# Kernel tuning notes

Hardware: AMD Instinct MI355X
Metric: run time of the kernel (lower is better)

The kernel has to match this reference:

```python
import jax, jax.numpy as jnp
import numpy as np

N = 50000
IN_CHNL = 128
OUT_CHNL = 64
HEADS = 2
NEG_SLOPE = 0.2  # PyG GATConv default leaky_relu slope


def gat_conv(x, W, a_src, a_dst, bias, edge_index):
    """PyG-style GATConv (concat=True, add_self_loops=True, eval mode).
    x: [N, F_in], W: [F_in, H*C], a_src/a_dst: [H, C], bias: [H*C],
    edge_index: [2, E] (row 0 = src, row 1 = dst)."""
    n = x.shape[0]
    loops = jnp.arange(n, dtype=edge_index.dtype)
    src = jnp.concatenate([edge_index[0], loops])
    dst = jnp.concatenate([edge_index[1], loops])

    h = (x @ W).reshape(n, HEADS, OUT_CHNL)          # [N, H, C]
    s_src = jnp.einsum('nhc,hc->nh', h, a_src)       # [N, H]
    s_dst = jnp.einsum('nhc,hc->nh', h, a_dst)       # [N, H]

    e = s_src[src] + s_dst[dst]                      # [E', H]
    e = jax.nn.leaky_relu(e, NEG_SLOPE)
    # segment softmax over destination neighborhoods
    e_max = jax.ops.segment_max(e, dst, num_segments=n)
    e_max = jnp.where(jnp.isfinite(e_max), e_max, 0.0)
    e_exp = jnp.exp(e - e_max[dst])
    denom = jax.ops.segment_sum(e_exp, dst, num_segments=n)
    alpha = e_exp / denom[dst]                       # [E', H]

    msg = h[src] * alpha[:, :, None]                 # [E', H, C]
    out = jax.ops.segment_sum(msg, dst, num_segments=n)  # [N, H, C]
    return out.reshape(n, HEADS * OUT_CHNL) + bias


def setup_inputs() -> dict:
    key = jax.random.key(0)
    ks = jax.random.split(key, 12)
    node_h = jax.random.normal(ks[0], (N, IN_CHNL), dtype=jnp.float32)
    edge_index_pc = jax.random.randint(ks[1], (2, 600000), 0, N, dtype=jnp.int64 if jax.config.jax_enable_x64 else jnp.int32)
    edge_index_mc = jax.random.randint(ks[2], (2, 600000), 0, N, dtype=jnp.int64 if jax.config.jax_enable_x64 else jnp.int32)
    sc = 1.0 / np.sqrt(IN_CHNL)
    W_pc = jax.random.normal(ks[3], (IN_CHNL, HEADS * OUT_CHNL), dtype=jnp.float32) * sc
    a_src_pc = jax.random.normal(ks[4], (HEADS, OUT_CHNL), dtype=jnp.float32) * sc
    a_dst_pc = jax.random.normal(ks[5], (HEADS, OUT_CHNL), dtype=jnp.float32) * sc
    b_pc = jnp.zeros((HEADS * OUT_CHNL,), dtype=jnp.float32)
    W_mc = jax.random.normal(ks[6], (IN_CHNL, HEADS * OUT_CHNL), dtype=jnp.float32) * sc
    a_src_mc = jax.random.normal(ks[7], (HEADS, OUT_CHNL), dtype=jnp.float32) * sc
    a_dst_mc = jax.random.normal(ks[8], (HEADS, OUT_CHNL), dtype=jnp.float32) * sc
    b_mc = jnp.zeros((HEADS * OUT_CHNL,), dtype=jnp.float32)
    return {
        'node_h': node_h,
        'W_pc': W_pc, 'a_src_pc': a_src_pc, 'a_dst_pc': a_dst_pc, 'b_pc': b_pc,
        'W_mc': W_mc, 'a_src_mc': a_src_mc, 'a_dst_mc': a_dst_mc, 'b_mc': b_mc,
        'edge_index_pc': edge_index_pc, 'edge_index_mc': edge_index_mc,
    }


def reference(node_h, W_pc, a_src_pc, a_dst_pc, b_pc,
              W_mc, a_src_mc, a_dst_mc, b_mc,
              edge_index_pc, edge_index_mc):
    # eval mode: F.dropout is identity
    h_pc = jax.nn.elu(gat_conv(node_h, W_pc, a_src_pc, a_dst_pc, b_pc, edge_index_pc))
    h_mc = jax.nn.elu(gat_conv(node_h, W_mc, a_src_mc, a_dst_mc, b_mc, edge_index_mc))
    return 0.5 * (h_pc + h_mc)
```

## Files before the change

### kernel.cpp

```cpp
#include <hip/hip_runtime.h>
#include <hip/hip_bf16.h>

typedef unsigned int u32;
typedef unsigned short u16;
typedef long long i64;
typedef __bf16 bf16x8 __attribute__((ext_vector_type(8)));
typedef float f32x4 __attribute__((ext_vector_type(4)));

static constexpr int NN = 50000;
static constexpr int FI = 128;
static constexpr int FO = 128;
static constexpr int ER = 600000;
static constexpr int GLAB = 6272;
static constexpr int PROWS = 12544;
static constexpr int DSTRIDE = 38;
static constexpr int NQA = 640;
static constexpr int ACS = (2 * ER) / NQA;
static constexpr int NBIN = 128;
static constexpr int RBLK = 784;
static constexpr int LCAP = 64;
static constexpr int QCAPB = 10240;
static constexpr float SLOPE = 0.2f;

__device__ __forceinline__ float bf2f(u16 u) {
  u32 x = ((u32)u) << 16;
  return __builtin_bit_cast(float, x);
}
__device__ __forceinline__ u16 f2bf(float f) {
  u32 u = __builtin_bit_cast(u32, f);
  u32 r = (u + 0x7fffu + ((u >> 16) & 1u)) >> 16;
  return (u16)r;
}
__device__ __forceinline__ float ldf(const void* p, size_t i, int isf32) {
  return isf32 ? ((const float*)p)[i] : bf2f(((const u16*)p)[i]);
}
__device__ __forceinline__ int lde(const void* p, size_t i, int is64) {
  return is64 ? (int)((const i64*)p)[i] : ((const int*)p)[i];
}

__global__ void wfrag_prep(const void* __restrict__ W0,
                           const void* __restrict__ W1,
                           const u32* __restrict__ x,
                           const u32* __restrict__ ei, u16* __restrict__ wf,
                           int* __restrict__ flags, int* __restrict__ qcur) {
  int lane = threadIdx.x;
  u32 e = (x[lane] >> 23) & 0xffu;
  unsigned long long b1 = __ballot(e >= 118u && e <= 137u);
  int f32i = (__popcll(b1) >= 48) ? 1 : 0;
  int bid = blockIdx.x;
  if (bid == 64) {
    if (lane < 64) {
      u32 hi = (lane < 32) ? ei[2 * lane + 1] : 1u;
      unsigned long long b2 = __ballot(hi == 0u);
      if (lane == 0) {
        flags[0] = f32i;
        flags[1] = (__popcll(b2) >= 30) ? 1 : 0;
      }
    }
    if (lane < NBIN - 64) qcur[64 + lane] = 0;
    if (lane < 64) qcur[lane] = 0;
    return;
  }
  int g = bid >> 5, idx = bid & 31;
  const void* W = g ? W1 : W0;
  int ks = idx >> 3, cg = idx & 7;
  int k0 = ks * 32 + (lane >> 4) * 8;
  int col = cg * 16 + (lane & 15);
  u16 v[8];
#pragma unroll
  for (int j = 0; j < 8; j++) v[j] = f2bf(ldf(W, (size_t)(k0 + j) * FO + col, f32i));
  u32 p0 = (u32)v[0] | ((u32)v[1] << 16);
  u32 p1 = (u32)v[2] | ((u32)v[3] << 16);
  u32 p2 = (u32)v[4] | ((u32)v[5] << 16);
  u32 p3 = (u32)v[6] | ((u32)v[7] << 16);
  *reinterpret_cast<uint4*>(wf + (size_t)(bid * 64 + lane) * 8) =
      make_uint4(p0, p1, p2, p3);
}

__device__ __forceinline__ void gemm_body(
    const void* __restrict__ x, const u16* __restrict__ wf,
    u16* __restrict__ h0, u16* __restrict__ h1, const void* __restrict__ as0,
    const void* __restrict__ ad0, const void* __restrict__ as1,
    const void* __restrict__ ad1, float* __restrict__ ss,
    float* __restrict__ sd, int f32i, int bid) {
  int tid = threadIdx.x;
  int lane = tid & 63;
  int wv = tid >> 6;
  int rowbase = bid * 64 + wv * 16;
  int arow = rowbase + (lane & 15);
  if (arow >= NN) arow = NN - 1;
  int kg = lane >> 4;

  f32x4 acc[16];
#pragma unroll
  for (int i = 0; i < 16; i++) acc[i] = (f32x4){0.f, 0.f, 0.f, 0.f};

#pragma unroll
  for (int ks = 0; ks < 4; ks++) {
    uint4 q;
    if (f32i) {
      const float* xp = (const float*)x + (size_t)arow * FI + ks * 32 + kg * 8;
      float4 v0 = *reinterpret_cast<const float4*>(xp);
      float4 v1 = *reinterpret_cast<const float4*>(xp + 4);
      q.x = (u32)f2bf(v0.x) | ((u32)f2bf(v0.y) << 16);
      q.y = (u32)f2bf(v0.z) | ((u32)f2bf(v0.w) << 16);
      q.z = (u32)f2bf(v1.x) | ((u32)f2bf(v1.y) << 16);
      q.w = (u32)f2bf(v1.z) | ((u32)f2bf(v1.w) << 16);
    } else {
      q = *reinterpret_cast<const uint4*>((const u16*)x + (size_t)arow * FI +
                                          ks * 32 + kg * 8);
    }
    bf16x8 a = __builtin_bit_cast(bf16x8, q);
#pragma unroll
    for (int cg = 0; cg < 16; cg++) {
      int g = cg >> 3;
      bf16x8 b = __builtin_bit_cast(
          bf16x8,
          *reinterpret_cast<const uint4*>(
              wf + (size_t)((g * 32 + ks * 8 + (cg & 7)) * 64 + lane) * 8));
      acc[cg] = __builtin_amdgcn_mfma_f32_16x16x32_bf16(a, b, acc[cg], 0, 0, 0);
    }
  }
#pragma unroll
  for (int cg = 0; cg < 16; cg++) {
    u16* h = (cg < 8) ? h0 : h1;
#pragma unroll
    for (int r = 0; r < 4; r++) {
      int orow = rowbase + kg * 4 + r;
      if (orow < NN)
        h[(size_t)orow * FO + (cg & 7) * 16 + (lane & 15)] = f2bf(acc[cg][r]);
    }
  }
  float sa[4][4], sb[4][4];
#pragma unroll
  for (int i = 0; i < 4; i++)
#pragma unroll
    for (int r = 0; r < 4; r++) {
      sa[i][r] = 0.f;
      sb[i][r] = 0.f;
    }
#pragma unroll
  for (int cg = 0; cg < 16; cg++) {
    int c = (cg & 7) * 16 + (lane & 15);
    const void* as = (cg < 8) ? as0 : as1;
    const void* ad = (cg < 8) ? ad0 : ad1;
    float av = ldf(as, c, f32i);
    float dv = ldf(ad, c, f32i);
    int ih = cg >> 2;
#pragma unroll
    for (int r = 0; r < 4; r++) {
      sa[ih][r] += acc[cg][r] * av;
      sb[ih][r] += acc[cg][r] * dv;
    }
  }
#pragma unroll
  for (int i = 0; i < 4; i++)
#pragma unroll
    for (int r = 0; r < 4; r++)
#pragma unroll
      for (int off = 1; off <= 8; off <<= 1) {
        sa[i][r] += __shfl_xor(sa[i][r], off, 64);
        sb[i][r] += __shfl_xor(sb[i][r], off, 64);
      }
  if ((lane & 15) < 8) {
    int r = lane & 3;
    int g = (lane >> 2) & 1;
    int row = rowbase + kg * 4 + r;
    if (row < NN) {
      reinterpret_cast<float2*>(ss)[(size_t)g * NN + row] =
          make_float2(sa[g * 2][r], sa[g * 2 + 1][r]);
      reinterpret_cast<float2*>(sd)[(size_t)g * NN + row] =
          make_float2(sb[g * 2][r], sb[g * 2 + 1][r]);
    }
  }
}

__device__ __forceinline__ void passA_body(const void* __restrict__ ei0,
                                           const void* __restrict__ ei1,
                                           int* __restrict__ qcur,
                                           u32* __restrict__ qbuf,
                                           const int* __restrict__ flags,
                                           int bid) {
  __shared__ u32 lq[NBIN][LCAP];
  __shared__ int lcnt[NBIN];
  __shared__ int gbase[NBIN];
  int tid = threadIdx.x;
  if (tid < NBIN) lcnt[tid] = 0;
  __syncthreads();
  int i64f = flags[1];
  int beg = bid * ACS;
  int end = beg + ACS;
  for (int e = beg + tid; e < end; e += 256) {
    int g = e >= ER;
    int ee = e - g * ER;
    const void* ei = g ? ei1 : ei0;
    int d = lde(ei, (size_t)ER + ee, i64f);
    int s = lde(ei, (size_t)ee, i64f);
    s = min(max(s, 0), NN - 1);
    d = min(max(d, 0), NN - 1);
    int p = d & 7;
    int label = (d >> 3) + g * GLAB;
    int r = label / RBLK;
    int bin = p * 16 + r;
    int ll = label - r * RBLK;
    int pos = atomicAdd(&lcnt[bin], 1);
    if (pos < LCAP) lq[bin][pos] = ((u32)s << 16) | (u32)ll;
  }
  __syncthreads();
  if (tid < NBIN) {
    int n = min(lcnt[tid], LCAP);
    lcnt[tid] = n;
    gbase[tid] = atomicAdd(&qcur[tid], n);
  }
  __syncthreads();
  int wv = tid >> 6, lane = tid & 63;
  for (int b = wv; b < NBIN; b += 4) {
    int n = lcnt[b];
    int gb = gbase[b];
    for (int i = lane; i < n; i += 64) {
      int idx = gb + i;
      if (idx < QCAPB) qbuf[(size_t)b * QCAPB + idx] = lq[b][i];
    }
  }
}

__global__ __launch_bounds__(256) void fat1(
    const void* __restrict__ x, const u16* __restrict__ wf,
    u16* __restrict__ h0, u16* __restrict__ h1, const void* __restrict__ as0,
    const void* __restrict__ ad0, const void* __restrict__ as1,
    const void* __restrict__ ad1, float* __restrict__ ss,
    float* __restrict__ sd, const void* __restrict__ ei0,
    const void* __restrict__ ei1, int* __restrict__ qcur,
    u32* __restrict__ qbuf, const int* __restrict__ flags) {
  if (blockIdx.x < NQA) {
    passA_body(ei0, ei1, qcur, qbuf, flags, blockIdx.x);
  } else {
    gemm_body(x, wf, h0, h1, as0, ad0, as1, ad1, ss, sd, flags[0],
              blockIdx.x - NQA);
  }
}

__global__ __launch_bounds__(256) void passB(const int* __restrict__ qcur,
                                             const u32* __restrict__ qbuf,
                                             int* __restrict__ deg,
                                             u16* __restrict__ slots) {
  __shared__ int ldeg[RBLK];
  __shared__ u16 lslots[RBLK * DSTRIDE];
  int tid = threadIdx.x;
  int bin = blockIdx.x;
  int p = bin >> 4, r = bin & 15;
  for (int i = tid; i < RBLK; i += 256) {
    int lgl = r * RBLK + i;
    int g = lgl >= GLAB;
    int lg = lgl - g * GLAB;
    int dst = (lg << 3) | p;
    if (dst < NN) {
      ldeg[i] = 1;
      lslots[i * DSTRIDE] = (u16)dst;
    } else {
      ldeg[i] = 0;
    }
  }
  __syncthreads();
  int qn = min(qcur[bin], QCAPB);
  const u32* q = qbuf + (size_t)bin * QCAPB;
  for (int i = tid; i < qn; i += 256) {
    u32 pr = q[i];
    int ll = (int)(pr & 0xffffu);
    int old = atomicAdd(&ldeg[ll], 1);
    if (old < DSTRIDE) lslots[ll * DSTRIDE + old] = (u16)(pr >> 16);
  }
  __syncthreads();
  int rowbase = p * PROWS + r * RBLK;
  for (int i = tid; i < RBLK; i += 256) deg[rowbase + i] = min(ldeg[i], DSTRIDE);
  const u32* ls32 = reinterpret_cast<const u32*>(lslots);
  u32* gs32 = reinterpret_cast<u32*>(slots + (size_t)rowbase * DSTRIDE);
  for (int i = tid; i < RBLK * DSTRIDE / 2; i += 256) gs32[i] = ls32[i];
}

__global__ __launch_bounds__(256) void agg2(
    const u16* __restrict__ h0, const u16* __restrict__ h1,
    const float* __restrict__ ss, const float* __restrict__ sd,
    const int* __restrict__ deg, const u16* __restrict__ slots,
    const void* __restrict__ b0p, const void* __restrict__ b1p,
    void* __restrict__ outp, const int* __restrict__ flags) {
  int f32i = flags[0];
  int tid = threadIdx.x;
  int lane = tid & 63, wv = tid >> 6;
  int half = lane >> 5;
  int c = lane & 31;
  int dst = blockIdx.x * 8 + wv * 2 + half;
  int head = c >> 4;
  int hsh = head << 4;
  int hbase = half << 5;
  float res[2][4];
#pragma unroll
  for (int g = 0; g < 2; g++) {
    const uint2* hw = reinterpret_cast<const uint2*>(g ? h1 : h0);
    const float2* ss2 = reinterpret_cast<const float2*>(ss) + (size_t)g * NN;
    float2 sdv = reinterpret_cast<const float2*>(sd)[(size_t)g * NN + dst];
    int row = (dst & 7) * PROWS + g * GLAB + (dst >> 3);
    int n = min(deg[row], DSTRIDE);
    const u16* srow = slots + (size_t)row * DSTRIDE;
    int n1 = min(n, 32);
    int s1 = 0, s2 = 0;
    u32 pp1 = 0, pp2 = 0;
    float dp0 = 0.f, dp1 = 0.f;
    if (c < n1) {
      s1 = srow[c];
      float2 sv = ss2[s1];
      float e0 = sv.x + sdv.x, e1 = sv.y + sdv.y;
      e0 = (e0 > 0.f) ? e0 : SLOPE * e0;
      e1 = (e1 > 0.f) ? e1 : SLOPE * e1;
      float q0 = __expf(e0), q1 = __expf(e1);
      pp1 = (u32)f2bf(q0) | ((u32)f2bf(q1) << 16);
      dp0 += q0;
      dp1 += q1;
    }
    if (c + 32 < n) {
      s2 = srow[c + 32];
      float2 sv = ss2[s2];
      float e0 = sv.x + sdv.x, e1 = sv.y + sdv.y;
      e0 = (e0 > 0.f) ? e0 : SLOPE * e0;
      e1 = (e1 > 0.f) ? e1 : SLOPE * e1;
      float q0 = __expf(e0), q1 = __expf(e1);
      pp2 = (u32)f2bf(q0) | ((u32)f2bf(q1) << 16);
      dp0 += q0;
      dp1 += q1;
    }
#pragma unroll
    for (int off = 16; off >= 1; off >>= 1) {
      dp0 += __shfl_xor(dp0, off, 32);
      dp1 += __shfl_xor(dp1, off, 32);
    }
    float den = head ? dp1 : dp0;
    float a0 = 0.f, a1 = 0.f, a2 = 0.f, a3 = 0.f;
    int n1full = n1 & ~7;
    for (int b = 0; b < n1full; b += 8) {
      uint2 hv[8];
      float pv[8];
#pragma unroll
      for (int t = 0; t < 8; t++) {
        int sj = __shfl(s1, hbase + b + t, 64);
        u32 pp = __shfl(pp1, hbase + b + t, 64);
        pv[t] = bf2f((u16)(pp >> hsh));
        hv[t] = hw[(size_t)sj * 32 + c];
      }
#pragma unroll
      for (int t = 0; t < 8; t++) {
        a0 += pv[t] * bf2f((u16)hv[t].x);
        a1 += pv[t] * bf2f((u16)(hv[t].x >> 16));
        a2 += pv[t] * bf2f((u16)hv[t].y);
        a3 += pv[t] * bf2f((u16)(hv[t].y >> 16));
      }
    }
    if (n1full < n1) {
      uint2 hv[8];
      float pv[8];
#pragma unroll
      for (int t = 0; t < 8; t++) {
        int jj = (n1full + t < n1) ? (n1full + t) : n1full;
        int sj = __shfl(s1, hbase + jj, 64);
        u32 pp = __shfl(pp1, hbase + jj, 64);
        pv[t] = (n1full + t < n1) ? bf2f((u16)(pp >> hsh)) : 0.f;
        hv[t] = hw[(size_t)sj * 32 + c];
      }
#pragma unroll
      for (int t = 0; t < 8; t++) {
        a0 += pv[t] * bf2f((u16)hv[t].x);
        a1 += pv[t] * bf2f((u16)(hv[t].x >> 16));
        a2 += pv[t] * bf2f((u16)hv[t].y);
        a3 += pv[t] * bf2f((u16)(hv[t].y >> 16));
      }
    }
    if (n > 32) {
      int n2 = n - 32;
      for (int b = 0; b < n2; b += 8) {
        uint2 hv[8];
        float pv[8];
#pragma unroll
        for (int t = 0; t < 8; t++) {
          int jj = (b + t < n2) ? (b + t) : b;
          int sj = __shfl(s2, hbase + jj, 64);
          u32 pp = __shfl(pp2, hbase + jj, 64);
          pv[t] = (b + t < n2) ? bf2f((u16)(pp >> hsh)) : 0.f;
          hv[t] = hw[(size_t)sj * 32 + c];
        }
#pragma unroll
        for (int t = 0; t < 8; t++) {
          a0 += pv[t] * bf2f((u16)hv[t].x);
          a1 += pv[t] * bf2f((u16)(hv[t].x >> 16));
          a2 += pv[t] * bf2f((u16)hv[t].y);
          a3 += pv[t] * bf2f((u16)(hv[t].y >> 16));
        }
      }
    }
    float inv = (den > 0.f) ? 1.0f / den : 0.f;
    const void* bias = g ? b1p : b0p;
    float r0 = a0 * inv + ldf(bias, 4 * c + 0, f32i);
    float r1 = a1 * inv + ldf(bias, 4 * c + 1, f32i);
    float r2 = a2 * inv + ldf(bias, 4 * c + 2, f32i);
    float r3 = a3 * inv + ldf(bias, 4 * c + 3, f32i);
    res[g][0] = (r0 > 0.f) ? r0 : (__expf(r0) - 1.0f);
    res[g][1] = (r1 > 0.f) ? r1 : (__expf(r1) - 1.0f);
    res[g][2] = (r2 > 0.f) ? r2 : (__expf(r2) - 1.0f);
    res[g][3] = (r3 > 0.f) ? r3 : (__expf(r3) - 1.0f);
  }
  float r0 = 0.5f * (res[0][0] + res[1][0]);
  float r1 = 0.5f * (res[0][1] + res[1][1]);
  float r2 = 0.5f * (res[0][2] + res[1][2]);
  float r3 = 0.5f * (res[0][3] + res[1][3]);
  if (f32i) {
    reinterpret_cast<float4*>(outp)[(size_t)dst * 32 + c] =
        make_float4(r0, r1, r2, r3);
  } else {
    uint2 o;
    o.x = (u32)f2bf(r0) | ((u32)f2bf(r1) << 16);
    o.y = (u32)f2bf(r2) | ((u32)f2bf(r3) << 16);
    reinterpret_cast<uint2*>(outp)[(size_t)dst * 32 + c] = o;
  }
}

extern "C" void kernel_launch(void* const* d_in, const int* in_sizes, int n_in,
                              void* d_out, int out_size, void* d_ws, size_t ws_size,
                              hipStream_t stream) {
  (void)in_sizes; (void)n_in; (void)out_size; (void)ws_size;
  const void* x = d_in[0];

  char* base = (char*)d_ws;
  size_t off = 0;
  auto alloc = [&](size_t bytes) -> void* {
    void* p = base + off;
    off = (off + bytes + 255) & ~(size_t)255;
    return p;
  };
  int* flags = (int*)alloc(16);
  int* qcur  = (int*)alloc(NBIN * 4);
  u16* h0    = (u16*)alloc((size_t)NN * FO * 2);
  u16* h1    = (u16*)alloc((size_t)NN * FO * 2);
  float* ss  = (float*)alloc((size_t)2 * NN * 2 * 4);
  float* sd  = (float*)alloc((size_t)2 * NN * 2 * 4);
  u16* wf    = (u16*)alloc((size_t)2 * 32 * 64 * 8 * 2);
  int* deg   = (int*)alloc((size_t)8 * PROWS * 4);
  u16* slots = (u16*)alloc((size_t)8 * PROWS * DSTRIDE * 2);
  u32* qbuf  = (u32*)alloc((size_t)NBIN * QCAPB * 4);

  const int GEMM_BLK = (NN + 63) / 64;
  const int AGG_BLK = NN / 8;

  wfrag_prep<<<65, 64, 0, stream>>>(d_in[1], d_in[5], (const u32*)x,
                                    (const u32*)d_in[9], wf, flags, qcur);
  fat1<<<NQA + GEMM_BLK, 256, 0, stream>>>(x, wf, h0, h1, d_in[2], d_in[3],
                                           d_in[6], d_in[7], ss, sd, d_in[9],
                                           d_in[10], qcur, qbuf, flags);
  passB<<<NBIN, 256, 0, stream>>>(qcur, qbuf, deg, slots);
  agg2<<<AGG_BLK, 256, 0, stream>>>(h0, h1, ss, sd, deg, slots, d_in[4],
                                    d_in[8], d_out, flags);
}
```

Measured before the change: 130.7 us.

## Restructure pre-aggregation stages: merge weight prep with edge binning, split GEMM per layer

Weight-fragment prep and the edge-binning pass now share one launch, so binning no longer depends on a prior flag kernel. The GEMM moves to its own launch with one block per layer per row tile, which halves accumulator registers per block and doubles block count. Edge binning uses twice as many blocks and a smaller per-block shared queue, with overflow going straight to global atomics. The per-bin counters are padded to separate cache lines and cleared by a memset. The trade-off is an extra kernel launch and a memset in exchange for better occupancy and less counter contention.

```diff
diff --git a/kernel.cpp b/kernel.cpp
--- a/kernel.cpp
+++ b/kernel.cpp
@@ -14,12 +14,13 @@
 static constexpr int GLAB = 6272;
 static constexpr int PROWS = 12544;
 static constexpr int DSTRIDE = 38;
-static constexpr int NQA = 640;
-static constexpr int ACS = (2 * ER) / NQA;
+static constexpr int NQA = 1280;
+static constexpr int ACS = (2 * ER + NQA - 1) / NQA;
 static constexpr int NBIN = 128;
 static constexpr int RBLK = 784;
-static constexpr int LCAP = 64;
+static constexpr int LCAP = 24;
 static constexpr int QCAPB = 10240;
+static constexpr int GEMM_BLK = (NN + 63) / 64;
 static constexpr float SLOPE = 0.2f;
 
 __device__ __forceinline__ float bf2f(u16 u) {
@@ -38,62 +39,128 @@
   return is64 ? (int)((const i64*)p)[i] : ((const int*)p)[i];
 }
 
-__global__ void wfrag_prep(const void* __restrict__ W0,
-                           const void* __restrict__ W1,
-                           const u32* __restrict__ x,
-                           const u32* __restrict__ ei, u16* __restrict__ wf,
-                           int* __restrict__ flags, int* __restrict__ qcur) {
-  int lane = threadIdx.x;
-  u32 e = (x[lane] >> 23) & 0xffu;
-  unsigned long long b1 = __ballot(e >= 118u && e <= 137u);
-  int f32i = (__popcll(b1) >= 48) ? 1 : 0;
+__device__ __forceinline__ void passA_body(const void* __restrict__ ei0,
+                                           const void* __restrict__ ei1,
+                                           int* __restrict__ qcurp,
+                                           u32* __restrict__ qbuf, int bid) {
+  __shared__ u32 lq[NBIN][LCAP];
+  __shared__ int lcnt[NBIN];
+  __shared__ int gbase[NBIN];
+  __shared__ int s_i64;
+  int tid = threadIdx.x;
+  if (tid < NBIN) lcnt[tid] = 0;
+  if (tid < 64) {
+    u32 hi = (tid < 32) ? ((const u32*)ei0)[2 * tid + 1] : 1u;
+    unsigned long long b2 = __ballot(hi == 0u);
+    if (tid == 0) s_i64 = (__popcll(b2) >= 30) ? 1 : 0;
+  }
+  __syncthreads();
+  int i64f = s_i64;
+  int beg = bid * ACS;
+  int end = min(beg + ACS, 2 * ER);
+  for (int e = beg + tid; e < end; e += 256) {
+    int g = e >= ER;
+    int ee = e - g * ER;
+    const void* ei = g ? ei1 : ei0;
+    int d = lde(ei, (size_t)ER + ee, i64f);
+    int s = lde(ei, (size_t)ee, i64f);
+    s = min(max(s, 0), NN - 1);
+    d = min(max(d, 0), NN - 1);
+    int p = d & 7;
+    int label = (d >> 3) + g * GLAB;
+    int r = label / RBLK;
+    int bin = p * 16 + r;
+    int ll = label - r * RBLK;
+    u32 entry = ((u32)s << 16) | (u32)ll;
+    int pos = atomicAdd(&lcnt[bin], 1);
+    if (pos < LCAP) {
+      lq[bin][pos] = entry;
+    } else {
+      int idx = atomicAdd(&qcurp[bin * 16], 1);
+      if (idx < QCAPB) qbuf[(size_t)bin * QCAPB + idx] = entry;
+    }
+  }
+  __syncthreads();
+  if (tid < NBIN) {
+    int n = min(lcnt[tid], LCAP);
+    lcnt[tid] = n;
+    gbase[tid] = atomicAdd(&qcurp[tid * 16], n);
+  }
+  __syncthreads();
+  int wv = tid >> 6, lane = tid & 63;
+  for (int b = wv; b < NBIN; b += 4) {
+    int n = lcnt[b];
+    int gb = gbase[b];
+    for (int i = lane; i < n; i += 64) {
+      int idx = gb + i;
+      if (idx < QCAPB) qbuf[(size_t)b * QCAPB + idx] = lq[b][i];
+    }
+  }
+}
+
+__global__ __launch_bounds__(256) void k1(
+    const void* __restrict__ W0, const void* __restrict__ W1,
+    const u32* __restrict__ x32, const void* __restrict__ ei0,
+    const void* __restrict__ ei1, u16* __restrict__ wf,
+    int* __restrict__ flags, int* __restrict__ qcurp, u32* __restrict__ qbuf) {
   int bid = blockIdx.x;
-  if (bid == 64) {
-    if (lane < 64) {
-      u32 hi = (lane < 32) ? ei[2 * lane + 1] : 1u;
+  int tid = threadIdx.x;
+  if (bid < 16) {
+    int lane = tid & 63;
+    int chunk = bid * 4 + (tid >> 6);
+    u32 e = (x32[lane] >> 23) & 0xffu;
+    unsigned long long b1 = __ballot(e >= 118u && e <= 137u);
+    int f32i = (__popcll(b1) >= 48) ? 1 : 0;
+    int g = chunk >> 5, idx = chunk & 31;
+    const void* W = g ? W1 : W0;
+    int ks = idx >> 3, cg = idx & 7;
+    int k0 = ks * 32 + (lane >> 4) * 8;
+    int col = cg * 16 + (lane & 15);
+    u16 v[8];
+#pragma unroll
+    for (int j = 0; j < 8; j++)
+      v[j] = f2bf(ldf(W, (size_t)(k0 + j) * FO + col, f32i));
+    u32 p0 = (u32)v[0] | ((u32)v[1] << 16);
+    u32 p1 = (u32)v[2] | ((u32)v[3] << 16);
+    u32 p2 = (u32)v[4] | ((u32)v[5] << 16);
+    u32 p3 = (u32)v[6] | ((u32)v[7] << 16);
+    *reinterpret_cast<uint4*>(wf + (size_t)(chunk * 64 + lane) * 8) =
+        make_uint4(p0, p1, p2, p3);
+    if (bid == 0 && tid < 64) {
+      u32 hi = (tid < 32) ? ((const u32*)ei0)[2 * tid + 1] : 1u;
       unsigned long long b2 = __ballot(hi == 0u);
-      if (lane == 0) {
+      if (tid == 0) {
         flags[0] = f32i;
         flags[1] = (__popcll(b2) >= 30) ? 1 : 0;
       }
     }
-    if (lane < NBIN - 64) qcur[64 + lane] = 0;
-    if (lane < 64) qcur[lane] = 0;
     return;
   }
-  int g = bid >> 5, idx = bid & 31;
-  const void* W = g ? W1 : W0;
-  int ks = idx >> 3, cg = idx & 7;
-  int k0 = ks * 32 + (lane >> 4) * 8;
-  int col = cg * 16 + (lane & 15);
-  u16 v[8];
-#pragma unroll
-  for (int j = 0; j < 8; j++) v[j] = f2bf(ldf(W, (size_t)(k0 + j) * FO + col, f32i));
-  u32 p0 = (u32)v[0] | ((u32)v[1] << 16);
-  u32 p1 = (u32)v[2] | ((u32)v[3] << 16);
-  u32 p2 = (u32)v[4] | ((u32)v[5] << 16);
-  u32 p3 = (u32)v[6] | ((u32)v[7] << 16);
-  *reinterpret_cast<uint4*>(wf + (size_t)(bid * 64 + lane) * 8) =
-      make_uint4(p0, p1, p2, p3);
-}
-
-__device__ __forceinline__ void gemm_body(
+  passA_body(ei0, ei1, qcurp, qbuf, bid - 16);
+}
+
+__global__ __launch_bounds__(256) void gemm2(
     const void* __restrict__ x, const u16* __restrict__ wf,
     u16* __restrict__ h0, u16* __restrict__ h1, const void* __restrict__ as0,
     const void* __restrict__ ad0, const void* __restrict__ as1,
     const void* __restrict__ ad1, float* __restrict__ ss,
-    float* __restrict__ sd, int f32i, int bid) {
+    float* __restrict__ sd, const int* __restrict__ flags) {
+  int f32i = flags[0];
+  int g = blockIdx.x >= GEMM_BLK;
+  int bid = blockIdx.x - g * GEMM_BLK;
+  u16* h = g ? h1 : h0;
+  const void* as = g ? as1 : as0;
+  const void* ad = g ? ad1 : ad0;
   int tid = threadIdx.x;
-  int lane = tid & 63;
-  int wv = tid >> 6;
+  int lane = tid & 63, wv = tid >> 6;
   int rowbase = bid * 64 + wv * 16;
   int arow = rowbase + (lane & 15);
   if (arow >= NN) arow = NN - 1;
   int kg = lane >> 4;
 
-  f32x4 acc[16];
-#pragma unroll
-  for (int i = 0; i < 16; i++) acc[i] = (f32x4){0.f, 0.f, 0.f, 0.f};
+  f32x4 acc[8];
+#pragma unroll
+  for (int i = 0; i < 8; i++) acc[i] = (f32x4){0.f, 0.f, 0.f, 0.f};
 
 #pragma unroll
   for (int ks = 0; ks < 4; ks++) {
@@ -112,38 +179,33 @@
     }
     bf16x8 a = __builtin_bit_cast(bf16x8, q);
 #pragma unroll
-    for (int cg = 0; cg < 16; cg++) {
-      int g = cg >> 3;
+    for (int cg = 0; cg < 8; cg++) {
       bf16x8 b = __builtin_bit_cast(
-          bf16x8,
-          *reinterpret_cast<const uint4*>(
-              wf + (size_t)((g * 32 + ks * 8 + (cg & 7)) * 64 + lane) * 8));
+          bf16x8, *reinterpret_cast<const uint4*>(
+                      wf + (size_t)((g * 32 + ks * 8 + cg) * 64 + lane) * 8));
       acc[cg] = __builtin_amdgcn_mfma_f32_16x16x32_bf16(a, b, acc[cg], 0, 0, 0);
     }
   }
 #pragma unroll
-  for (int cg = 0; cg < 16; cg++) {
-    u16* h = (cg < 8) ? h0 : h1;
+  for (int cg = 0; cg < 8; cg++) {
 #pragma unroll
     for (int r = 0; r < 4; r++) {
       int orow = rowbase + kg * 4 + r;
       if (orow < NN)
-        h[(size_t)orow * FO + (cg & 7) * 16 + (lane & 15)] = f2bf(acc[cg][r]);
-    }
-  }
-  float sa[4][4], sb[4][4];
-#pragma unroll
-  for (int i = 0; i < 4; i++)
+        h[(size_t)orow * FO + cg * 16 + (lane & 15)] = f2bf(acc[cg][r]);
+    }
+  }
+  float sa[2][4], sb[2][4];
+#pragma unroll
+  for (int i = 0; i < 2; i++)
 #pragma unroll
     for (int r = 0; r < 4; r++) {
       sa[i][r] = 0.f;
       sb[i][r] = 0.f;
     }
 #pragma unroll
-  for (int cg = 0; cg < 16; cg++) {
-    int c = (cg & 7) * 16 + (lane & 15);
-    const void* as = (cg < 8) ? as0 : as1;
-    const void* ad = (cg < 8) ? ad0 : ad1;
+  for (int cg = 0; cg < 8; cg++) {
+    int c = cg * 16 + (lane & 15);
     float av = ldf(as, c, f32i);
     float dv = ldf(ad, c, f32i);
     int ih = cg >> 2;
@@ -154,7 +216,7 @@
     }
   }
 #pragma unroll
-  for (int i = 0; i < 4; i++)
+  for (int i = 0; i < 2; i++)
 #pragma unroll
     for (int r = 0; r < 4; r++)
 #pragma unroll
@@ -162,85 +224,19 @@
         sa[i][r] += __shfl_xor(sa[i][r], off, 64);
         sb[i][r] += __shfl_xor(sb[i][r], off, 64);
       }
-  if ((lane & 15) < 8) {
+  if ((lane & 15) < 4) {
     int r = lane & 3;
-    int g = (lane >> 2) & 1;
     int row = rowbase + kg * 4 + r;
     if (row < NN) {
       reinterpret_cast<float2*>(ss)[(size_t)g * NN + row] =
-          make_float2(sa[g * 2][r], sa[g * 2 + 1][r]);
+          make_float2(sa[0][r], sa[1][r]);
       reinterpret_cast<float2*>(sd)[(size_t)g * NN + row] =
-          make_float2(sb[g * 2][r], sb[g * 2 + 1][r]);
-    }
-  }
-}
-
-__device__ __forceinline__ void passA_body(const void* __restrict__ ei0,
-                                           const void* __restrict__ ei1,
-                                           int* __restrict__ qcur,
-                                           u32* __restrict__ qbuf,
-                                           const int* __restrict__ flags,
-                                           int bid) {
-  __shared__ u32 lq[NBIN][LCAP];
-  __shared__ int lcnt[NBIN];
-  __shared__ int gbase[NBIN];
-  int tid = threadIdx.x;
-  if (tid < NBIN) lcnt[tid] = 0;
-  __syncthreads();
-  int i64f = flags[1];
-  int beg = bid * ACS;
-  int end = beg + ACS;
-  for (int e = beg + tid; e < end; e += 256) {
-    int g = e >= ER;
-    int ee = e - g * ER;
-    const void* ei = g ? ei1 : ei0;
-    int d = lde(ei, (size_t)ER + ee, i64f);
-    int s = lde(ei, (size_t)ee, i64f);
-    s = min(max(s, 0), NN - 1);
-    d = min(max(d, 0), NN - 1);
-    int p = d & 7;
-    int label = (d >> 3) + g * GLAB;
-    int r = label / RBLK;
-    int bin = p * 16 + r;
-    int ll = label - r * RBLK;
-    int pos = atomicAdd(&lcnt[bin], 1);
-    if (pos < LCAP) lq[bin][pos] = ((u32)s << 16) | (u32)ll;
-  }
-  __syncthreads();
-  if (tid < NBIN) {
-    int n = min(lcnt[tid], LCAP);
-    lcnt[tid] = n;
-    gbase[tid] = atomicAdd(&qcur[tid], n);
-  }
-  __syncthreads();
-  int wv = tid >> 6, lane = tid & 63;
-  for (int b = wv; b < NBIN; b += 4) {
-    int n = lcnt[b];
-    int gb = gbase[b];
-    for (int i = lane; i < n; i += 64) {
-      int idx = gb + i;
-      if (idx < QCAPB) qbuf[(size_t)b * QCAPB + idx] = lq[b][i];
-    }
-  }
-}
-
-__global__ __launch_bounds__(256) void fat1(
-    const void* __restrict__ x, const u16* __restrict__ wf,
-    u16* __restrict__ h0, u16* __restrict__ h1, const void* __restrict__ as0,
-    const void* __restrict__ ad0, const void* __restrict__ as1,
-    const void* __restrict__ ad1, float* __restrict__ ss,
-    float* __restrict__ sd, const void* __restrict__ ei0,
-    const void* __restrict__ ei1, int* __restrict__ qcur,
-    u32* __restrict__ qbuf, const int* __restrict__ flags) {
-  if (blockIdx.x < NQA) {
-    passA_body(ei0, ei1, qcur, qbuf, flags, blockIdx.x);
-  } else {
-    gemm_body(x, wf, h0, h1, as0, ad0, as1, ad1, ss, sd, flags[0],
-              blockIdx.x - NQA);
-  }
-}
-
-__global__ __launch_bounds__(256) void passB(const int* __restrict__ qcur,
+          make_float2(sb[0][r], sb[1][r]);
+    }
+  }
+}
+
+__global__ __launch_bounds__(256) void passB(const int* __restrict__ qcurp,
                                              const u32* __restrict__ qbuf,
                                              int* __restrict__ deg,
                                              u16* __restrict__ slots) {
@@ -262,7 +258,7 @@
     }
   }
   __syncthreads();
-  int qn = min(qcur[bin], QCAPB);
+  int qn = min(qcurp[bin * 16], QCAPB);
   const u32* q = qbuf + (size_t)bin * QCAPB;
   for (int i = tid; i < qn; i += 256) {
     u32 pr = q[i];
@@ -435,7 +431,7 @@
     return p;
   };
   int* flags = (int*)alloc(16);
-  int* qcur  = (int*)alloc(NBIN * 4);
+  int* qcurp = (int*)alloc((size_t)NBIN * 16 * 4);
   u16* h0    = (u16*)alloc((size_t)NN * FO * 2);
   u16* h1    = (u16*)alloc((size_t)NN * FO * 2);
   float* ss  = (float*)alloc((size_t)2 * NN * 2 * 4);
@@ -445,15 +441,14 @@
   u16* slots = (u16*)alloc((size_t)8 * PROWS * DSTRIDE * 2);
   u32* qbuf  = (u32*)alloc((size_t)NBIN * QCAPB * 4);
 
-  const int GEMM_BLK = (NN + 63) / 64;
   const int AGG_BLK = NN / 8;
 
-  wfrag_prep<<<65, 64, 0, stream>>>(d_in[1], d_in[5], (const u32*)x,
-                                    (const u32*)d_in[9], wf, flags, qcur);
-  fat1<<<NQA + GEMM_BLK, 256, 0, stream>>>(x, wf, h0, h1, d_in[2], d_in[3],
-                                           d_in[6], d_in[7], ss, sd, d_in[9],
-                                           d_in[10], qcur, qbuf, flags);
-  passB<<<NBIN, 256, 0, stream>>>(qcur, qbuf, deg, slots);
+  hipMemsetAsync(qcurp, 0, (size_t)NBIN * 16 * 4, stream);
+  k1<<<16 + NQA, 256, 0, stream>>>(d_in[1], d_in[5], (const u32*)x, d_in[9],
+                                   d_in[10], wf, flags, qcurp, qbuf);
+  gemm2<<<2 * GEMM_BLK, 256, 0, stream>>>(x, wf, h0, h1, d_in[2], d_in[3],
+                                          d_in[6], d_in[7], ss, sd, flags);
+  passB<<<NBIN, 256, 0, stream>>>(qcurp, qbuf, deg, slots);
   agg2<<<AGG_BLK, 256, 0, stream>>>(h0, h1, ss, sd, deg, slots, d_in[4],
                                     d_in[8], d_out, flags);
 }
```

Result: slower. 141.6 us (+8.3%).
